# Performance work log

Measured on AMD Instinct MI355X. Metric: run time of the kernel, lower is better.

The kernel has to match this reference:

```python
import jax, jax.numpy as jnp
import numpy as np

D_MODEL = 1280
D_BOTTLE = 64
LN_EPS = 1e-5


def setup_inputs() -> dict:
    key = jax.random.key(0)
    k1, k2, k3, k4, k5 = jax.random.split(key, 5)
    x = jax.random.normal(k1, (16, 1500, D_MODEL), dtype=jnp.float32)
    # LayerNorm params (torch default: weight=1, bias=0; use random-ish gamma for a stronger test)
    gamma = jnp.ones((D_MODEL,), dtype=jnp.float32)
    beta = jnp.zeros((D_MODEL,), dtype=jnp.float32)
    # Linear weights stored torch-style: [out, in]
    w_down = jax.random.normal(k2, (D_BOTTLE, D_MODEL), dtype=jnp.float32) * (1.0 / np.sqrt(D_MODEL))
    b_down = jax.random.normal(k3, (D_BOTTLE,), dtype=jnp.float32) * 0.01
    # up_proj is zero-initialized in the module; use small random values so gradients/outputs are nontrivial
    w_up = jax.random.normal(k4, (D_MODEL, D_BOTTLE), dtype=jnp.float32) * 0.01
    b_up = jax.random.normal(k5, (D_MODEL,), dtype=jnp.float32) * 0.01
    return {"x": x, "gamma": gamma, "beta": beta, "w_down": w_down, "b_down": b_down, "w_up": w_up, "b_up": b_up}


def reference(x, gamma, beta, w_down, b_down, w_up, b_up):
    # LayerNorm over last dim
    mean = jnp.mean(x, axis=-1, keepdims=True)
    var = jnp.mean(jnp.square(x - mean), axis=-1, keepdims=True)
    h = (x - mean) * jax.lax.rsqrt(var + LN_EPS) * gamma + beta
    # down-proj -> GELU -> up-proj (torch GELU default = exact erf form)
    h = jnp.einsum('bsd,kd->bsk', h, w_down) + b_down   # [B,S,64]
    h = jax.nn.gelu(h, approximate=False)
    h = jnp.einsum('bsk,dk->bsd', h, w_up) + b_up       # [B,S,1280]
    return h + x
```

## Files before the change

kernel.cpp:

```cpp
#include <hip/hip_runtime.h>
#include <hip/hip_bf16.h>

#define D_MODEL  1280
#define D_BOTTLE 64
#define LN_EPS   1e-5f
#define TM       16
#define HP       1288
#define GP       72

typedef __attribute__((ext_vector_type(8))) short short8;
typedef __attribute__((ext_vector_type(4))) float floatx4;

static __device__ inline unsigned short f2bf(float f) {
    __hip_bfloat16 h = __float2bfloat16(f);
    return *reinterpret_cast<unsigned short*>(&h);
}

__global__ void convert_weights(const float* __restrict__ wd, const float* __restrict__ wu,
                                unsigned short* __restrict__ wd_b, unsigned short* __restrict__ wu_b) {
    int i = blockIdx.x * blockDim.x + threadIdx.x;
    if (i < D_MODEL * D_BOTTLE) {
        wd_b[i] = f2bf(wd[i]);
        wu_b[i] = f2bf(wu[i]);
    }
}

__global__ __launch_bounds__(256, 2) void adapter_kernel(
    const float* __restrict__ x,
    const float* __restrict__ gamma, const float* __restrict__ beta,
    const unsigned short* __restrict__ wd_b, const float* __restrict__ b_down,
    const unsigned short* __restrict__ wu_b, const float* __restrict__ b_up,
    float* __restrict__ out)
{
    __shared__ unsigned short h_lds[TM * HP];
    __shared__ unsigned short g_lds[TM * GP];

    const int tid  = threadIdx.x;
    const int wave = tid >> 6;
    const int lane = tid & 63;
    const int r0   = blockIdx.x * TM;

    const int rloc = wave * 4 + (lane >> 4);
    const int lr   = lane & 15;
    const float* xrow = x + (size_t)(r0 + rloc) * D_MODEL;

    float s = 0.f, sq = 0.f;
    #pragma unroll
    for (int t = 0; t < 20; ++t) {
        float4 v = *reinterpret_cast<const float4*>(xrow + (lr + 16 * t) * 4);
        s  += v.x + v.y + v.z + v.w;
        sq += v.x * v.x + v.y * v.y + v.z * v.z + v.w * v.w;
    }
    #pragma unroll
    for (int m = 1; m < 16; m <<= 1) {
        s  += __shfl_xor(s, m);
        sq += __shfl_xor(sq, m);
    }
    const float mean = s * (1.f / D_MODEL);
    const float var  = sq * (1.f / D_MODEL) - mean * mean;
    const float rinv = rsqrtf(var + LN_EPS);

    #pragma unroll
    for (int t = 0; t < 20; ++t) {
        const int c = (lr + 16 * t) * 4;
        float4 v  = *reinterpret_cast<const float4*>(xrow + c);
        float4 g4 = *reinterpret_cast<const float4*>(gamma + c);
        float4 b4 = *reinterpret_cast<const float4*>(beta + c);
        ushort4 pk;
        pk.x = f2bf((v.x - mean) * rinv * g4.x + b4.x);
        pk.y = f2bf((v.y - mean) * rinv * g4.y + b4.y);
        pk.z = f2bf((v.z - mean) * rinv * g4.z + b4.z);
        pk.w = f2bf((v.w - mean) * rinv * g4.w + b4.w);
        *reinterpret_cast<ushort4*>(&h_lds[rloc * HP + c]) = pk;
    }
    __syncthreads();

    const int l15   = lane & 15;
    const int khalf = lane >> 4;
    const int n0    = wave * 16;

    floatx4 acc = {0.f, 0.f, 0.f, 0.f};
    const unsigned short* arow = h_lds + l15 * HP + khalf * 8;
    const unsigned short* brow = wd_b + (size_t)(n0 + l15) * D_MODEL + khalf * 8;
    #pragma unroll 8
    for (int kk = 0; kk < 40; ++kk) {
        short8 a = *reinterpret_cast<const short8*>(arow + kk * 32);
        short8 b = *reinterpret_cast<const short8*>(brow + kk * 32);
        acc = __builtin_amdgcn_mfma_f32_16x16x32_bf16(a, b, acc, 0, 0, 0);
    }

    const float bd = b_down[n0 + l15];
    #pragma unroll
    for (int r = 0; r < 4; ++r) {
        const int m = khalf * 4 + r;
        const float yv = acc[r] + bd;
        const float gv = 0.5f * yv * (1.f + erff(yv * 0.70710678118654752f));
        g_lds[m * GP + n0 + l15] = f2bf(gv);
    }
    __syncthreads();

    short8 ga0 = *reinterpret_cast<const short8*>(g_lds + l15 * GP +  0 + khalf * 8);
    short8 ga1 = *reinterpret_cast<const short8*>(g_lds + l15 * GP + 32 + khalf * 8);

    const int m_base = khalf * 4;
    #pragma unroll 4
    for (int i = 0; i < 20; ++i) {
        const int d0 = (i * 4 + wave) * 16;
        const int d  = d0 + l15;
        const unsigned short* bptr = wu_b + (size_t)d * D_BOTTLE + khalf * 8;
        short8 b0 = *reinterpret_cast<const short8*>(bptr);
        short8 b1 = *reinterpret_cast<const short8*>(bptr + 32);
        floatx4 acc2 = {0.f, 0.f, 0.f, 0.f};
        acc2 = __builtin_amdgcn_mfma_f32_16x16x32_bf16(ga0, b0, acc2, 0, 0, 0);
        acc2 = __builtin_amdgcn_mfma_f32_16x16x32_bf16(ga1, b1, acc2, 0, 0, 0);
        const float bu = b_up[d];
        #pragma unroll
        for (int r = 0; r < 4; ++r) {
            const size_t idx = (size_t)(r0 + m_base + r) * D_MODEL + d;
            out[idx] = acc2[r] + bu + x[idx];
        }
    }
}

extern "C" void kernel_launch(void* const* d_in, const int* in_sizes, int n_in,
                              void* d_out, int out_size, void* d_ws, size_t ws_size,
                              hipStream_t stream) {
    const float* x      = (const float*)d_in[0];
    const float* gamma  = (const float*)d_in[1];
    const float* beta   = (const float*)d_in[2];
    const float* w_down = (const float*)d_in[3];
    const float* b_down = (const float*)d_in[4];
    const float* w_up   = (const float*)d_in[5];
    const float* b_up   = (const float*)d_in[6];
    float* out = (float*)d_out;

    unsigned short* wd_b = (unsigned short*)d_ws;
    unsigned short* wu_b = wd_b + D_MODEL * D_BOTTLE;

    convert_weights<<<(D_MODEL * D_BOTTLE + 255) / 256, 256, 0, stream>>>(w_down, w_up, wd_b, wu_b);

    const int rows = in_sizes[0] / D_MODEL;
    adapter_kernel<<<rows / TM, 256, 0, stream>>>(x, gamma, beta, wd_b, b_down, wu_b, b_up, out);
}
```

Before: 281.4 us.

## Fold LayerNorm into down-projection weights and drop normalized LDS tile

Folds gamma into the down-projection weights and beta into its bias, and applies mean and rstd after the matmul through a weight column-sum correction. The down GEMM now reads raw x from global memory, converting to bf16 in registers, instead of staging a normalized bf16 tile in LDS. This removes the large LDS buffer so the launch bound can request more blocks per SM, and removes the second normalization pass. In exchange, each wave rereads x rows from global/L2 during the GEMM, two small prep kernels are added, and quantizing raw x before centering may lose precision.

```diff
diff --git a/kernel.cpp b/kernel.cpp
--- a/kernel.cpp
+++ b/kernel.cpp
@@ -5,7 +5,6 @@
 #define D_BOTTLE 64
 #define LN_EPS   1e-5f
 #define TM       16
-#define HP       1288
 #define GP       72
 
 typedef __attribute__((ext_vector_type(8))) short short8;
@@ -15,24 +14,55 @@
     __hip_bfloat16 h = __float2bfloat16(f);
     return *reinterpret_cast<unsigned short*>(&h);
 }
+static __device__ inline float bf2f(unsigned short u) {
+    unsigned int v = ((unsigned int)u) << 16;
+    return __uint_as_float(v);
+}
 
-__global__ void convert_weights(const float* __restrict__ wd, const float* __restrict__ wu,
-                                unsigned short* __restrict__ wd_b, unsigned short* __restrict__ wu_b) {
+__global__ void prep_weights(const float* __restrict__ wd, const float* __restrict__ gamma,
+                             const float* __restrict__ wu,
+                             unsigned short* __restrict__ wg, unsigned short* __restrict__ wu_b) {
     int i = blockIdx.x * blockDim.x + threadIdx.x;
     if (i < D_MODEL * D_BOTTLE) {
-        wd_b[i] = f2bf(wd[i]);
+        int k = i % D_MODEL;
+        wg[i]   = f2bf(wd[i] * gamma[k]);
         wu_b[i] = f2bf(wu[i]);
     }
 }
 
-__global__ __launch_bounds__(256, 2) void adapter_kernel(
+__global__ void prep_reduce(const unsigned short* __restrict__ wg, const float* __restrict__ wd,
+                            const float* __restrict__ beta, const float* __restrict__ b_down,
+                            float* __restrict__ colsum, float* __restrict__ bd2) {
+    const int n = blockIdx.x;
+    const int t = threadIdx.x;
+    float cs = 0.f, bb = 0.f;
+    for (int k = t; k < D_MODEL; k += 256) {
+        cs += bf2f(wg[n * D_MODEL + k]);
+        bb += wd[n * D_MODEL + k] * beta[k];
+    }
+    #pragma unroll
+    for (int m = 1; m < 64; m <<= 1) {
+        cs += __shfl_xor(cs, m);
+        bb += __shfl_xor(bb, m);
+    }
+    __shared__ float scs[4], sbb[4];
+    if ((t & 63) == 0) { scs[t >> 6] = cs; sbb[t >> 6] = bb; }
+    __syncthreads();
+    if (t == 0) {
+        colsum[n] = scs[0] + scs[1] + scs[2] + scs[3];
+        bd2[n]    = b_down[n] + sbb[0] + sbb[1] + sbb[2] + sbb[3];
+    }
+}
+
+__global__ __launch_bounds__(256, 4) void adapter_kernel(
     const float* __restrict__ x,
-    const float* __restrict__ gamma, const float* __restrict__ beta,
-    const unsigned short* __restrict__ wd_b, const float* __restrict__ b_down,
+    const unsigned short* __restrict__ wg, const float* __restrict__ colsum,
+    const float* __restrict__ bd2,
     const unsigned short* __restrict__ wu_b, const float* __restrict__ b_up,
     float* __restrict__ out)
 {
-    __shared__ unsigned short h_lds[TM * HP];
+    __shared__ float s_mean[TM];
+    __shared__ float s_rinv[TM];
     __shared__ unsigned short g_lds[TM * GP];
 
     const int tid  = threadIdx.x;
@@ -40,62 +70,64 @@
     const int lane = tid & 63;
     const int r0   = blockIdx.x * TM;
 
-    const int rloc = wave * 4 + (lane >> 4);
-    const int lr   = lane & 15;
-    const float* xrow = x + (size_t)(r0 + rloc) * D_MODEL;
-
-    float s = 0.f, sq = 0.f;
-    #pragma unroll
-    for (int t = 0; t < 20; ++t) {
-        float4 v = *reinterpret_cast<const float4*>(xrow + (lr + 16 * t) * 4);
-        s  += v.x + v.y + v.z + v.w;
-        sq += v.x * v.x + v.y * v.y + v.z * v.z + v.w * v.w;
-    }
-    #pragma unroll
-    for (int m = 1; m < 16; m <<= 1) {
-        s  += __shfl_xor(s, m);
-        sq += __shfl_xor(sq, m);
-    }
-    const float mean = s * (1.f / D_MODEL);
-    const float var  = sq * (1.f / D_MODEL) - mean * mean;
-    const float rinv = rsqrtf(var + LN_EPS);
-
-    #pragma unroll
-    for (int t = 0; t < 20; ++t) {
-        const int c = (lr + 16 * t) * 4;
-        float4 v  = *reinterpret_cast<const float4*>(xrow + c);
-        float4 g4 = *reinterpret_cast<const float4*>(gamma + c);
-        float4 b4 = *reinterpret_cast<const float4*>(beta + c);
-        ushort4 pk;
-        pk.x = f2bf((v.x - mean) * rinv * g4.x + b4.x);
-        pk.y = f2bf((v.y - mean) * rinv * g4.y + b4.y);
-        pk.z = f2bf((v.z - mean) * rinv * g4.z + b4.z);
-        pk.w = f2bf((v.w - mean) * rinv * g4.w + b4.w);
-        *reinterpret_cast<ushort4*>(&h_lds[rloc * HP + c]) = pk;
+    {
+        const int rloc = wave * 4 + (lane >> 4);
+        const int lr   = lane & 15;
+        const float* xrow = x + (size_t)(r0 + rloc) * D_MODEL;
+        float s = 0.f, sq = 0.f;
+        #pragma unroll
+        for (int t = 0; t < 20; ++t) {
+            float4 v = *reinterpret_cast<const float4*>(xrow + (lr + 16 * t) * 4);
+            s  += v.x + v.y + v.z + v.w;
+            sq += v.x * v.x + v.y * v.y + v.z * v.z + v.w * v.w;
+        }
+        #pragma unroll
+        for (int m = 1; m < 16; m <<= 1) {
+            s  += __shfl_xor(s, m);
+            sq += __shfl_xor(sq, m);
+        }
+        const float mean = s * (1.f / D_MODEL);
+        const float var  = sq * (1.f / D_MODEL) - mean * mean;
+        if (lr == 0) {
+            s_mean[rloc] = mean;
+            s_rinv[rloc] = rsqrtf(var + LN_EPS);
+        }
     }
     __syncthreads();
 
     const int l15   = lane & 15;
     const int khalf = lane >> 4;
     const int n0    = wave * 16;
+    const int nn    = n0 + l15;
 
     floatx4 acc = {0.f, 0.f, 0.f, 0.f};
-    const unsigned short* arow = h_lds + l15 * HP + khalf * 8;
-    const unsigned short* brow = wd_b + (size_t)(n0 + l15) * D_MODEL + khalf * 8;
-    #pragma unroll 8
-    for (int kk = 0; kk < 40; ++kk) {
-        short8 a = *reinterpret_cast<const short8*>(arow + kk * 32);
-        short8 b = *reinterpret_cast<const short8*>(brow + kk * 32);
-        acc = __builtin_amdgcn_mfma_f32_16x16x32_bf16(a, b, acc, 0, 0, 0);
+    {
+        const float* arow = x + (size_t)(r0 + l15) * D_MODEL + khalf * 8;
+        const unsigned short* brow = wg + (size_t)nn * D_MODEL + khalf * 8;
+        #pragma unroll 4
+        for (int kk = 0; kk < 40; ++kk) {
+            float4 a0 = *reinterpret_cast<const float4*>(arow + kk * 32);
+            float4 a1 = *reinterpret_cast<const float4*>(arow + kk * 32 + 4);
+            short8 a;
+            a[0] = (short)f2bf(a0.x); a[1] = (short)f2bf(a0.y);
+            a[2] = (short)f2bf(a0.z); a[3] = (short)f2bf(a0.w);
+            a[4] = (short)f2bf(a1.x); a[5] = (short)f2bf(a1.y);
+            a[6] = (short)f2bf(a1.z); a[7] = (short)f2bf(a1.w);
+            short8 b = *reinterpret_cast<const short8*>(brow + kk * 32);
+            acc = __builtin_amdgcn_mfma_f32_16x16x32_bf16(a, b, acc, 0, 0, 0);
+        }
     }
 
-    const float bd = b_down[n0 + l15];
-    #pragma unroll
-    for (int r = 0; r < 4; ++r) {
-        const int m = khalf * 4 + r;
-        const float yv = acc[r] + bd;
-        const float gv = 0.5f * yv * (1.f + erff(yv * 0.70710678118654752f));
-        g_lds[m * GP + n0 + l15] = f2bf(gv);
+    {
+        const float cs  = colsum[nn];
+        const float bdn = bd2[nn];
+        #pragma unroll
+        for (int r = 0; r < 4; ++r) {
+            const int m = khalf * 4 + r;
+            const float yv = s_rinv[m] * (acc[r] - s_mean[m] * cs) + bdn;
+            const float gv = 0.5f * yv * (1.f + erff(yv * 0.70710678118654752f));
+            g_lds[m * GP + nn] = f2bf(gv);
+        }
     }
     __syncthreads();
 
@@ -134,11 +166,14 @@
     const float* b_up   = (const float*)d_in[6];
     float* out = (float*)d_out;
 
-    unsigned short* wd_b = (unsigned short*)d_ws;
-    unsigned short* wu_b = wd_b + D_MODEL * D_BOTTLE;
+    unsigned short* wg   = (unsigned short*)d_ws;
+    unsigned short* wu_b = wg + D_MODEL * D_BOTTLE;
+    float* colsum = (float*)(wu_b + D_MODEL * D_BOTTLE);
+    float* bd2    = colsum + D_BOTTLE;
 
-    convert_weights<<<(D_MODEL * D_BOTTLE + 255) / 256, 256, 0, stream>>>(w_down, w_up, wd_b, wu_b);
+    prep_weights<<<(D_MODEL * D_BOTTLE + 255) / 256, 256, 0, stream>>>(w_down, gamma, w_up, wg, wu_b);
+    prep_reduce<<<D_BOTTLE, 256, 0, stream>>>(wg, w_down, beta, b_down, colsum, bd2);
 
     const int rows = in_sizes[0] / D_MODEL;
-    adapter_kernel<<<rows / TM, 256, 0, stream>>>(x, gamma, beta, wd_b, b_down, wu_b, b_up, out);
+    adapter_kernel<<<rows / TM, 256, 0, stream>>>(x, wg, colsum, bd2, wu_b, b_up, out);
 }
```

After: 331.4 us. +17.8%, slower.
